# Kernel tuning notes

Measured on AMD Instinct MI355X. Metric: run time of the kernel, lower is better.

Reference implementation:

```python
import jax, jax.numpy as jnp
import numpy as np

EPS = 1e-7


def setup_inputs() -> dict:
    key = jax.random.key(0)
    k1, k2 = jax.random.split(key)
    N, C = 16384, 10000
    pred = jax.random.normal(k1, (N, C), dtype=jnp.float32)
    labels = jax.random.randint(k2, (N,), 0, C)
    return {"pred": pred, "labels": labels}


def reference(pred, labels):
    N, C = pred.shape
    # randomness of the torch module (random negative offsets + np.random.rand gate),
    # made deterministic/on-device with a fixed key
    k_off, k_u = jax.random.split(jax.random.key(42))
    offsets = jax.random.randint(k_off, (N,), 1, C)          # random_(1, C)
    rand_u = jax.random.uniform(k_u, (N,), dtype=jnp.float32)  # np.random.rand per sample

    target_neg = (labels + offsets) % C                       # shifted-label negatives

    norms = jnp.linalg.norm(pred, axis=-1, keepdims=True) + EPS  # [N,1]
    logit_norm = pred / norms / 2.0
    snorm = jax.nn.softmax(logit_norm, axis=1) + EPS          # [N,C]
    log_snorm = jnp.log(snorm)

    max_prob = jnp.max(snorm, axis=1)                         # argmax_snorm[0]
    argmax = jnp.argmax(snorm, axis=1)                        # argmax_snorm[1]
    # vectorized form of the per-sample loop: replace negative with argmax class
    replace = (rand_u <= max_prob) & (argmax != labels)
    target_neg = jnp.where(replace, argmax, target_neg)

    rows = jnp.arange(N)
    # (1 - onehot(labels)) * log_snorm summed == full row sum minus label entry
    pos_term = (log_snorm.sum(axis=1) - log_snorm[rows, labels]).mean()
    neg_term = log_snorm[rows, target_neg].mean()
    loss = 10.0 * (pos_term - neg_term)
    return (loss, jnp.squeeze(norms))
```

## Files before the change

### kernel.cpp

```cpp
#include <hip/hip_runtime.h>
#include <stdint.h>

#define NROWS 16384
#define NC    10000
#define NF4   (NC / 4)
#define BLK   512
#define KMAX  ((NF4 + BLK - 1) / BLK)
#define NWAVE (BLK / 64)
#define EPSF  1e-7f

__device__ __forceinline__ void tf2x32(uint32_t k0, uint32_t k1,
                                       uint32_t x0, uint32_t x1,
                                       uint32_t& o0, uint32_t& o1) {
  const uint32_t ks2 = k0 ^ k1 ^ 0x1BD11BDAu;
  uint32_t v0 = x0 + k0, v1 = x1 + k1;
#define TF_R(r) { v0 += v1; v1 = (v1 << (r)) | (v1 >> (32 - (r))); v1 ^= v0; }
  TF_R(13) TF_R(15) TF_R(26) TF_R(6)
  v0 += k1;  v1 += ks2 + 1u;
  TF_R(17) TF_R(29) TF_R(16) TF_R(24)
  v0 += ks2; v1 += k0 + 2u;
  TF_R(13) TF_R(15) TF_R(26) TF_R(6)
  v0 += k0;  v1 += k1 + 3u;
  TF_R(17) TF_R(29) TF_R(16) TF_R(24)
  v0 += k1;  v1 += ks2 + 4u;
  TF_R(13) TF_R(15) TF_R(26) TF_R(6)
  v0 += ks2; v1 += k0 + 5u;
#undef TF_R
  o0 = v0; o1 = v1;
}

__global__ __launch_bounds__(BLK, 8)
void nnce_row_kernel(const float* __restrict__ pred,
                     const int* __restrict__ labels,
                     float* __restrict__ out,
                     float* __restrict__ row_acc)
{
  __shared__ float r_ss[NWAVE], r_sp[NWAVE], r_mv[NWAVE], r_z[NWAVE];
  __shared__ int   r_mi[NWAVE];
  __shared__ float bcast[1];

  const int row  = blockIdx.x;
  const int tid  = threadIdx.x;
  const int lane = tid & 63;
  const int wid  = tid >> 6;
  const float* p = pred + (size_t)row * NC;
  const float4* p4 = (const float4*)p;

  float4 v[KMAX];
  float ss = 0.f, sp = 0.f, mv = -1e30f;
  int mi = 0;
#pragma unroll
  for (int k = 0; k < KMAX; ++k) {
    const int idx = tid + k * BLK;
    if (idx < NF4) {
      const float4 t = p4[idx];
      v[k] = t;
      ss += t.x * t.x + t.y * t.y + t.z * t.z + t.w * t.w;
      sp += t.x + t.y + t.z + t.w;
      const int b = 4 * idx;
      if (t.x > mv) { mv = t.x; mi = b;     }
      if (t.y > mv) { mv = t.y; mi = b + 1; }
      if (t.z > mv) { mv = t.z; mi = b + 2; }
      if (t.w > mv) { mv = t.w; mi = b + 3; }
    }
  }
  for (int off = 32; off > 0; off >>= 1) {
    ss += __shfl_down(ss, off, 64);
    sp += __shfl_down(sp, off, 64);
    float om = __shfl_down(mv, off, 64);
    int   oi = __shfl_down(mi, off, 64);
    if (om > mv || (om == mv && oi < mi)) { mv = om; mi = oi; }
  }
  if (lane == 0) { r_ss[wid] = ss; r_sp[wid] = sp; r_mv[wid] = mv; r_mi[wid] = mi; }
  __syncthreads();
  if (tid == 0) {
    float tss = r_ss[0], tsp = r_sp[0], tmv = r_mv[0];
    int   tmi = r_mi[0];
    for (int w = 1; w < NWAVE; ++w) {
      tss += r_ss[w]; tsp += r_sp[w];
      if (r_mv[w] > tmv || (r_mv[w] == tmv && r_mi[w] < tmi)) { tmv = r_mv[w]; tmi = r_mi[w]; }
    }
    const float norm = sqrtf(tss) + EPSF;
    out[1 + row] = norm;
    bcast[0] = 0.5f / norm;
    r_sp[0] = tsp;
    r_mv[0] = tmv;
    r_mi[0] = tmi;
  }
  __syncthreads();
  const float inv2n = bcast[0];

  float zl = 0.f;
#pragma unroll
  for (int k = 0; k < KMAX; ++k) {
    const int idx = tid + k * BLK;
    if (idx < NF4) {
      const float4 t = v[k];
      zl += __expf(t.x * inv2n) + __expf(t.y * inv2n)
          + __expf(t.z * inv2n) + __expf(t.w * inv2n);
    }
  }
  for (int off = 32; off > 0; off >>= 1) zl += __shfl_down(zl, off, 64);
  if (lane == 0) r_z[wid] = zl;
  __syncthreads();

  if (tid == 0) {
    float Z = 0.f;
    for (int w = 0; w < NWAVE; ++w) Z += r_z[w];
    const float sumx = r_sp[0] * inv2n;
    const float pmax = r_mv[0];
    const int   amax = r_mi[0];
    const int   lab  = labels[row];
    const float logZ = logf(Z);
    const float eZ   = EPSF * Z;

    uint32_t a0, a1, b0, b1;
    tf2x32(0u, 42u, 0u, 0u, a0, a1);
    tf2x32(0u, 42u, 0u, 1u, b0, b1);
    uint32_t h0, h1, lo0, lo1, u0, u1;
    tf2x32(a0, a1, 0u, (uint32_t)row,            h0,  h1);
    tf2x32(a0, a1, 0u, (uint32_t)(NROWS + row),  lo0, lo1);
    tf2x32(b0, b1, 0u, (uint32_t)row,            u0,  u1);
    const uint32_t span = 9999u, mult = 6835u;
    uint32_t off = ((h1 % span) * mult + (lo1 % span)) % span;
    const int   offset = 1 + (int)off;
    const float ru = __uint_as_float((u1 >> 9) | 0x3F800000u) - 1.0f;

    int tneg = (lab + offset) % NC;
    const float max_prob = __expf(pmax * inv2n) / Z + EPSF;
    if (ru <= max_prob && amax != lab) tneg = amax;

    const float x_lab = p[lab]  * inv2n;
    const float x_neg = p[tneg] * inv2n;
    const float ls_lab = x_lab + eZ * __expf(-x_lab) - logZ;
    const float ls_neg = x_neg + eZ * __expf(-x_neg) - logZ;
    const float sumlog = sumx - (float)NC * logZ;

    row_acc[row] = (sumlog - ls_lab) - ls_neg;
  }
}

__global__ __launch_bounds__(BLK)
void nnce_loss_kernel(const float* __restrict__ row_acc, float* __restrict__ out) {
  __shared__ double red[BLK];
  double s = 0.0;
  for (int i = threadIdx.x; i < NROWS; i += BLK) s += (double)row_acc[i];
  red[threadIdx.x] = s;
  __syncthreads();
  for (int k = BLK / 2; k > 0; k >>= 1) {
    if (threadIdx.x < k) red[threadIdx.x] += red[threadIdx.x + k];
    __syncthreads();
  }
  if (threadIdx.x == 0) out[0] = (float)(10.0 * red[0] / (double)NROWS);
}

extern "C" void kernel_launch(void* const* d_in, const int* in_sizes, int n_in,
                              void* d_out, int out_size, void* d_ws, size_t ws_size,
                              hipStream_t stream) {
  const float* pred   = (const float*)d_in[0];
  const int*   labels = (const int*)d_in[1];
  float* out = (float*)d_out;
  float* row_acc = (float*)d_ws;

  nnce_row_kernel<<<NROWS, BLK, 0, stream>>>(pred, labels, out, row_acc);
  nnce_loss_kernel<<<1, BLK, 0, stream>>>(row_acc, out);
}
```

Baseline: 134.8 us.

## Process 32 rows per block with double-buffered register prefetch of next rows

Measured after the change: 147.0 us. +9.0%, slower.

```diff
diff --git a/kernel.cpp b/kernel.cpp
--- a/kernel.cpp
+++ b/kernel.cpp
@@ -5,13 +5,16 @@
 #define NC    10000
 #define NF4   (NC / 4)
 #define BLK   512
-#define KMAX  ((NF4 + BLK - 1) / BLK)
+#define KMAX  5
 #define NWAVE (BLK / 64)
+#define RPB   32
+#define NBLK  (NROWS / RPB)
 #define EPSF  1e-7f
 
-__device__ __forceinline__ void tf2x32(uint32_t k0, uint32_t k1,
-                                       uint32_t x0, uint32_t x1,
-                                       uint32_t& o0, uint32_t& o1) {
+struct U2 { uint32_t a, b; };
+
+__host__ __device__ constexpr U2 tf2x32(uint32_t k0, uint32_t k1,
+                                        uint32_t x0, uint32_t x1) {
   const uint32_t ks2 = k0 ^ k1 ^ 0x1BD11BDAu;
   uint32_t v0 = x0 + k0, v1 = x1 + k1;
 #define TF_R(r) { v0 += v1; v1 = (v1 << (r)) | (v1 >> (32 - (r))); v1 ^= v0; }
@@ -26,35 +29,65 @@
   TF_R(13) TF_R(15) TF_R(26) TF_R(6)
   v0 += ks2; v1 += k0 + 5u;
 #undef TF_R
-  o0 = v0; o1 = v1;
-}
-
-__global__ __launch_bounds__(BLK, 8)
-void nnce_row_kernel(const float* __restrict__ pred,
-                     const int* __restrict__ labels,
-                     float* __restrict__ out,
-                     float* __restrict__ row_acc)
-{
-  __shared__ float r_ss[NWAVE], r_sp[NWAVE], r_mv[NWAVE], r_z[NWAVE];
-  __shared__ int   r_mi[NWAVE];
-  __shared__ float bcast[1];
-
-  const int row  = blockIdx.x;
+  return {v0, v1};
+}
+
+constexpr U2 KA = tf2x32(0u, 42u, 0u, 0u);
+constexpr U2 KB = tf2x32(0u, 42u, 0u, 1u);
+
+__device__ __forceinline__ void bsync() {
+  asm volatile("s_waitcnt lgkmcnt(0)" ::: "memory");
+  __builtin_amdgcn_s_barrier();
+  asm volatile("" ::: "memory");
+}
+
+__device__ __forceinline__ void load_row(float4 (&buf)[KMAX], const float4* p4) {
+#pragma unroll
+  for (int k = 0; k < KMAX; ++k) {
+    const int idx = threadIdx.x + k * BLK;
+    if (idx < NF4) buf[k] = p4[idx];
+  }
+}
+
+struct Red {
+  float r_ss[NWAVE], r_sp[NWAVE], r_mv[NWAVE], r_z[NWAVE];
+  int   r_mi[NWAVE];
+  float inv2n;
+};
+
+__device__ __forceinline__ double process_row(float4 (&buf)[KMAX],
+                                              const float* __restrict__ pred,
+                                              const int* __restrict__ labels,
+                                              float* __restrict__ out,
+                                              Red& S, int row, int pfrow,
+                                              bool do_pf) {
   const int tid  = threadIdx.x;
   const int lane = tid & 63;
   const int wid  = tid >> 6;
-  const float* p = pred + (size_t)row * NC;
-  const float4* p4 = (const float4*)p;
-
-  float4 v[KMAX];
+
+  int lab = 0, cand1 = 0;
+  float p_lab = 0.f, p_c1 = 0.f, ru = 0.f;
+  if (tid == 0) {
+    lab = labels[row];
+    const U2 h  = tf2x32(KA.a, KA.b, 0u, (uint32_t)row);
+    const U2 lo = tf2x32(KA.a, KA.b, 0u, (uint32_t)(NROWS + row));
+    const U2 uu = tf2x32(KB.a, KB.b, 0u, (uint32_t)row);
+    const uint32_t span = 9999u, mult = 6835u;
+    const uint32_t off = ((h.b % span) * mult + (lo.b % span)) % span;
+    ru = __uint_as_float((uu.b >> 9) | 0x3F800000u) - 1.0f;
+    cand1 = (lab + 1 + (int)off) % NC;
+    const float* p = pred + (size_t)row * NC;
+    p_lab = p[lab];
+    p_c1  = p[cand1];
+  }
+
   float ss = 0.f, sp = 0.f, mv = -1e30f;
   int mi = 0;
 #pragma unroll
   for (int k = 0; k < KMAX; ++k) {
     const int idx = tid + k * BLK;
     if (idx < NF4) {
-      const float4 t = p4[idx];
-      v[k] = t;
+      const float4 t = buf[k];
       ss += t.x * t.x + t.y * t.y + t.z * t.z + t.w * t.w;
       sp += t.x + t.y + t.z + t.w;
       const int b = 4 * idx;
@@ -71,80 +104,94 @@
     int   oi = __shfl_down(mi, off, 64);
     if (om > mv || (om == mv && oi < mi)) { mv = om; mi = oi; }
   }
-  if (lane == 0) { r_ss[wid] = ss; r_sp[wid] = sp; r_mv[wid] = mv; r_mi[wid] = mi; }
-  __syncthreads();
+  if (lane == 0) { S.r_ss[wid] = ss; S.r_sp[wid] = sp; S.r_mv[wid] = mv; S.r_mi[wid] = mi; }
+  bsync();
   if (tid == 0) {
-    float tss = r_ss[0], tsp = r_sp[0], tmv = r_mv[0];
-    int   tmi = r_mi[0];
+    float tss = S.r_ss[0], tsp = S.r_sp[0], tmv = S.r_mv[0];
+    int   tmi = S.r_mi[0];
     for (int w = 1; w < NWAVE; ++w) {
-      tss += r_ss[w]; tsp += r_sp[w];
-      if (r_mv[w] > tmv || (r_mv[w] == tmv && r_mi[w] < tmi)) { tmv = r_mv[w]; tmi = r_mi[w]; }
+      tss += S.r_ss[w]; tsp += S.r_sp[w];
+      if (S.r_mv[w] > tmv || (S.r_mv[w] == tmv && S.r_mi[w] < tmi)) {
+        tmv = S.r_mv[w]; tmi = S.r_mi[w];
+      }
     }
     const float norm = sqrtf(tss) + EPSF;
     out[1 + row] = norm;
-    bcast[0] = 0.5f / norm;
-    r_sp[0] = tsp;
-    r_mv[0] = tmv;
-    r_mi[0] = tmi;
-  }
-  __syncthreads();
-  const float inv2n = bcast[0];
+    S.inv2n  = 0.5f / norm;
+    S.r_sp[0] = tsp;
+    S.r_mv[0] = tmv;
+    S.r_mi[0] = tmi;
+  }
+  bsync();
+  const float inv2n = S.inv2n;
 
   float zl = 0.f;
 #pragma unroll
   for (int k = 0; k < KMAX; ++k) {
     const int idx = tid + k * BLK;
     if (idx < NF4) {
-      const float4 t = v[k];
+      const float4 t = buf[k];
       zl += __expf(t.x * inv2n) + __expf(t.y * inv2n)
           + __expf(t.z * inv2n) + __expf(t.w * inv2n);
     }
   }
+  if (do_pf) load_row(buf, (const float4*)(pred + (size_t)pfrow * NC));
+
   for (int off = 32; off > 0; off >>= 1) zl += __shfl_down(zl, off, 64);
-  if (lane == 0) r_z[wid] = zl;
-  __syncthreads();
-
+  if (lane == 0) S.r_z[wid] = zl;
+  bsync();
+
+  double val = 0.0;
   if (tid == 0) {
     float Z = 0.f;
-    for (int w = 0; w < NWAVE; ++w) Z += r_z[w];
-    const float sumx = r_sp[0] * inv2n;
-    const float pmax = r_mv[0];
-    const int   amax = r_mi[0];
-    const int   lab  = labels[row];
+    for (int w = 0; w < NWAVE; ++w) Z += S.r_z[w];
+    const float sumx = S.r_sp[0] * inv2n;
+    const float pmax = S.r_mv[0];
+    const int   amax = S.r_mi[0];
     const float logZ = logf(Z);
     const float eZ   = EPSF * Z;
 
-    uint32_t a0, a1, b0, b1;
-    tf2x32(0u, 42u, 0u, 0u, a0, a1);
-    tf2x32(0u, 42u, 0u, 1u, b0, b1);
-    uint32_t h0, h1, lo0, lo1, u0, u1;
-    tf2x32(a0, a1, 0u, (uint32_t)row,            h0,  h1);
-    tf2x32(a0, a1, 0u, (uint32_t)(NROWS + row),  lo0, lo1);
-    tf2x32(b0, b1, 0u, (uint32_t)row,            u0,  u1);
-    const uint32_t span = 9999u, mult = 6835u;
-    uint32_t off = ((h1 % span) * mult + (lo1 % span)) % span;
-    const int   offset = 1 + (int)off;
-    const float ru = __uint_as_float((u1 >> 9) | 0x3F800000u) - 1.0f;
-
-    int tneg = (lab + offset) % NC;
     const float max_prob = __expf(pmax * inv2n) / Z + EPSF;
-    if (ru <= max_prob && amax != lab) tneg = amax;
-
-    const float x_lab = p[lab]  * inv2n;
-    const float x_neg = p[tneg] * inv2n;
+    const bool  replace  = (ru <= max_prob) && (amax != lab);
+    const float p_neg = replace ? pmax : p_c1;
+
+    const float x_lab = p_lab * inv2n;
+    const float x_neg = p_neg * inv2n;
     const float ls_lab = x_lab + eZ * __expf(-x_lab) - logZ;
     const float ls_neg = x_neg + eZ * __expf(-x_neg) - logZ;
     const float sumlog = sumx - (float)NC * logZ;
 
-    row_acc[row] = (sumlog - ls_lab) - ls_neg;
-  }
+    val = (double)((sumlog - ls_lab) - ls_neg);
+  }
+  return val;
+}
+
+__global__ __launch_bounds__(BLK, 4)
+void nnce_rows(const float* __restrict__ pred,
+               const int* __restrict__ labels,
+               float* __restrict__ out,
+               float* __restrict__ partial)
+{
+  __shared__ Red S;
+  const int r0 = blockIdx.x * RPB;
+
+  float4 bufA[KMAX], bufB[KMAX];
+  load_row(bufA, (const float4*)(pred + (size_t)r0 * NC));
+  load_row(bufB, (const float4*)(pred + (size_t)(r0 + 1) * NC));
+
+  double acc = 0.0;
+#pragma unroll 1
+  for (int i = 0; i < RPB; i += 2) {
+    acc += process_row(bufA, pred, labels, out, S, r0 + i,     r0 + i + 2, i + 2 < RPB);
+    acc += process_row(bufB, pred, labels, out, S, r0 + i + 1, r0 + i + 3, i + 3 < RPB);
+  }
+  if (threadIdx.x == 0) partial[blockIdx.x] = (float)acc;
 }
 
 __global__ __launch_bounds__(BLK)
-void nnce_loss_kernel(const float* __restrict__ row_acc, float* __restrict__ out) {
+void nnce_final(const float* __restrict__ partial, float* __restrict__ out) {
   __shared__ double red[BLK];
-  double s = 0.0;
-  for (int i = threadIdx.x; i < NROWS; i += BLK) s += (double)row_acc[i];
+  double s = (threadIdx.x < NBLK) ? (double)partial[threadIdx.x] : 0.0;
   red[threadIdx.x] = s;
   __syncthreads();
   for (int k = BLK / 2; k > 0; k >>= 1) {
@@ -159,9 +206,9 @@
                               hipStream_t stream) {
   const float* pred   = (const float*)d_in[0];
   const int*   labels = (const int*)d_in[1];
-  float* out = (float*)d_out;
-  float* row_acc = (float*)d_ws;
-
-  nnce_row_kernel<<<NROWS, BLK, 0, stream>>>(pred, labels, out, row_acc);
-  nnce_loss_kernel<<<1, BLK, 0, stream>>>(row_acc, out);
-}
+  float* out     = (float*)d_out;
+  float* partial = (float*)d_ws;
+
+  nnce_rows<<<NBLK, BLK, 0, stream>>>(pred, labels, out, partial);
+  nnce_final<<<1, BLK, 0, stream>>>(partial, out);
+}
```
